# Kernel optimization log

Hardware: AMD Instinct MI355X
Metric: run time of the kernel (lower is better)

The kernel has to match this reference:

```python
import jax, jax.numpy as jnp
import numpy as np

D_MODEL = 1024
NUM_HEADS = 16
D_K = D_MODEL // NUM_HEADS
LN_EPS = 1e-5


def setup_inputs() -> dict:
    key = jax.random.key(0)
    ks = jax.random.split(key, 13)
    B, S, D = 2, 2048, D_MODEL
    s = 1.0 / np.sqrt(D)
    return {
        "query": jax.random.normal(ks[0], (B, S, D), jnp.float32),
        "key": jax.random.normal(ks[1], (B, S, D), jnp.float32),
        "value": jax.random.normal(ks[2], (B, S, D), jnp.float32),
        "Wq": jax.random.normal(ks[3], (D, D), jnp.float32) * s,
        "bq": jnp.zeros((D,), jnp.float32),
        "Wk": jax.random.normal(ks[4], (D, D), jnp.float32) * s,
        "bk": jnp.zeros((D,), jnp.float32),
        "Wv": jax.random.normal(ks[5], (D, D), jnp.float32) * s,
        "bv": jnp.zeros((D,), jnp.float32),
        "Wo": jax.random.normal(ks[6], (D, D), jnp.float32) * s,
        "bo": jnp.zeros((D,), jnp.float32),
        "gamma": jnp.ones((D,), jnp.float32),
        "beta": jnp.zeros((D,), jnp.float32),
    }


def _mha(query, key, value, Wq, bq, Wk, bk, Wv, bv, Wo, bo, gamma, beta):
    B, S, D = query.shape
    H, dk = NUM_HEADS, D_K
    # projections (x @ W + b), reshape to [B, H, S, dk]
    Q = (query @ Wq + bq).reshape(B, S, H, dk).transpose(0, 2, 1, 3)
    K = (key @ Wk + bk).reshape(B, S, H, dk).transpose(0, 2, 1, 3)
    V = (value @ Wv + bv).reshape(B, S, H, dk).transpose(0, 2, 1, 3)
    scores = jnp.einsum("bhsd,bhtd->bhst", Q, K) / np.sqrt(dk).astype(np.float32)
    attn = jax.nn.softmax(scores, axis=-1)  # dropout is identity at inference
    ctx = jnp.einsum("bhst,bhtd->bhsd", attn, V)
    ctx = ctx.transpose(0, 2, 1, 3).reshape(B, S, D)
    out = ctx @ Wo + bo
    # residual + LayerNorm
    x = out + query
    mu = jnp.mean(x, axis=-1, keepdims=True)
    var = jnp.mean(jnp.square(x - mu), axis=-1, keepdims=True)
    y = (x - mu) / jnp.sqrt(var + LN_EPS) * gamma + beta
    return y, attn


def reference(query, key, value, Wq, bq, Wk, bk, Wv, bv, Wo, bo, gamma, beta):
    return _mha(query, key, value, Wq, bq, Wk, bk, Wv, bv, Wo, bo, gamma, beta)
```

## Files before the change

kernel.cpp:

```cpp
#include <hip/hip_runtime.h>
#include <stdint.h>

typedef __attribute__((ext_vector_type(8))) short bf16x8;
typedef __attribute__((ext_vector_type(4))) float f32x4;
typedef unsigned short u16;

#define DEVINL static __device__ __forceinline__

namespace {
constexpr int kS = 2048, kD = 1024, kH = 16, kDK = 64;
constexpr int kBS = 4096, kBH = 32;
constexpr float kEps = 1e-5f;
constexpr float kQScale = 0.125f * 1.44269504088896340736f;
}

DEVINL u16 f2bf(float f) {
  union { float f; unsigned u; } v; v.f = f;
  unsigned r = v.u + 0x7fffu + ((v.u >> 16) & 1u);
  return (u16)(r >> 16);
}
DEVINL float bf2f(u16 us) {
  union { unsigned u; float f; } v; v.u = ((unsigned)us) << 16; return v.f;
}
DEVINL f32x4 mfma16(bf16x8 a, bf16x8 b, f32x4 c) {
  return __builtin_amdgcn_mfma_f32_16x16x32_bf16(a, b, c, 0, 0, 0);
}

__global__ __launch_bounds__(256, 4)
void k_cvt_x(const float* __restrict__ xq, const float* __restrict__ xk,
             const float* __restrict__ xv, u16* __restrict__ oq,
             u16* __restrict__ ok, u16* __restrict__ ov) {
  const int z = blockIdx.y;
  const float* __restrict__ src = (z == 0) ? xq : (z == 1) ? xk : xv;
  u16* __restrict__ dst = (z == 0) ? oq : (z == 1) ? ok : ov;
  const size_t idx = (size_t)blockIdx.x * 256 + threadIdx.x;
  const float4 a = *reinterpret_cast<const float4*>(&src[idx * 8]);
  const float4 b = *reinterpret_cast<const float4*>(&src[idx * 8 + 4]);
  u16 pk[8] = {f2bf(a.x), f2bf(a.y), f2bf(a.z), f2bf(a.w),
               f2bf(b.x), f2bf(b.y), f2bf(b.z), f2bf(b.w)};
  *reinterpret_cast<bf16x8*>(&dst[idx * 8]) =
      *reinterpret_cast<const bf16x8*>(pk);
}

__global__ __launch_bounds__(256, 4)
void k_cvt_w(const float* __restrict__ wq, const float* __restrict__ wk,
             const float* __restrict__ wv, const float* __restrict__ wo,
             u16* __restrict__ oq, u16* __restrict__ ok,
             u16* __restrict__ ov, u16* __restrict__ oo) {
  const int z = blockIdx.z;
  const float* __restrict__ W = (z == 0) ? wq : (z == 1) ? wk : (z == 2) ? wv : wo;
  u16* __restrict__ Wt = (z == 0) ? oq : (z == 1) ? ok : (z == 2) ? ov : oo;
  const int n0 = blockIdx.x * 64, k0 = blockIdx.y * 64;
  const int tid = threadIdx.x;
  __shared__ u16 Tl[64][65];
#pragma unroll
  for (int p = 0; p < 4; ++p) {
    const int idx = tid + p * 256;
    const int kr = idx >> 4, cg = (idx & 15) * 4;
    const float4 v = *reinterpret_cast<const float4*>(&W[(size_t)(k0 + kr) * kD + n0 + cg]);
    Tl[kr][cg + 0] = f2bf(v.x);
    Tl[kr][cg + 1] = f2bf(v.y);
    Tl[kr][cg + 2] = f2bf(v.z);
    Tl[kr][cg + 3] = f2bf(v.w);
  }
  __syncthreads();
  const int n = tid >> 2, kc = (tid & 3) * 16;
  u16 buf[16];
#pragma unroll
  for (int i = 0; i < 16; ++i) buf[i] = Tl[kc + i][n];
  *reinterpret_cast<bf16x8*>(&Wt[(size_t)(n0 + n) * kD + k0 + kc]) =
      *reinterpret_cast<const bf16x8*>(&buf[0]);
  *reinterpret_cast<bf16x8*>(&Wt[(size_t)(n0 + n) * kD + k0 + kc + 8]) =
      *reinterpret_cast<const bf16x8*>(&buf[8]);
}

__global__ __launch_bounds__(256, 2)
void k_proj(const u16* __restrict__ Xq, const u16* __restrict__ Xk,
            const u16* __restrict__ Xv, const u16* __restrict__ Wtq,
            const u16* __restrict__ Wtk, const u16* __restrict__ Wtv,
            const float* __restrict__ bq, const float* __restrict__ bk,
            const float* __restrict__ bv, u16* __restrict__ Qo,
            u16* __restrict__ Ko, u16* __restrict__ Vo) {
  const int which = blockIdx.z;
  const u16* __restrict__ X = (which == 0) ? Xq : (which == 1) ? Xk : Xv;
  const u16* __restrict__ Wt = (which == 0) ? Wtq : (which == 1) ? Wtk : Wtv;
  const float* __restrict__ bias = (which == 0) ? bq : (which == 1) ? bk : bv;
  const float os = (which == 0) ? kQScale : 1.0f;

  const int n0 = blockIdx.x * 128, m0 = blockIdx.y * 128;
  const int tid = threadIdx.x, w = tid >> 6, l = tid & 63;

  __shared__ u16 Al[128][72];
  __shared__ u16 Bl[128][72];

  f32x4 acc[2][8];
#pragma unroll
  for (int i = 0; i < 2; ++i)
#pragma unroll
    for (int j = 0; j < 8; ++j) acc[i][j] = f32x4{0.f, 0.f, 0.f, 0.f};

  for (int k0 = 0; k0 < kD; k0 += 64) {
    __syncthreads();
#pragma unroll
    for (int p = 0; p < 4; ++p) {
      const int idx = tid + p * 256;
      const int row = idx >> 3, c = (idx & 7) * 8;
      *reinterpret_cast<bf16x8*>(&Al[row][c]) =
          *reinterpret_cast<const bf16x8*>(&X[(size_t)(m0 + row) * kD + k0 + c]);
      *reinterpret_cast<bf16x8*>(&Bl[row][c]) =
          *reinterpret_cast<const bf16x8*>(&Wt[(size_t)(n0 + row) * kD + k0 + c]);
    }
    __syncthreads();
#pragma unroll
    for (int k0i = 0; k0i < 64; k0i += 32) {
      const int kk = k0i + (l >> 4) * 8;
      bf16x8 a[2], b[8];
#pragma unroll
      for (int mi = 0; mi < 2; ++mi)
        a[mi] = *reinterpret_cast<const bf16x8*>(&Al[w * 32 + mi * 16 + (l & 15)][kk]);
#pragma unroll
      for (int nj = 0; nj < 8; ++nj)
        b[nj] = *reinterpret_cast<const bf16x8*>(&Bl[nj * 16 + (l & 15)][kk]);
#pragma unroll
      for (int mi = 0; mi < 2; ++mi)
#pragma unroll
        for (int nj = 0; nj < 8; ++nj)
          acc[mi][nj] = mfma16(a[mi], b[nj], acc[mi][nj]);
    }
  }

  u16* __restrict__ Out = (which == 0) ? Qo : (which == 1) ? Ko : Vo;
#pragma unroll
  for (int mi = 0; mi < 2; ++mi)
#pragma unroll
    for (int nj = 0; nj < 8; ++nj) {
      const int col = n0 + nj * 16 + (l & 15);
      const int h = col >> 6, d = col & 63;
      const float bvv = bias[col];
      const int row0 = m0 + w * 32 + mi * 16 + (l >> 4) * 4;
      if (which == 2) {
        const int b_ = row0 >> 11, s0 = row0 & 2047;
        alignas(8) u16 pk[4];
#pragma unroll
        for (int r = 0; r < 4; ++r) pk[r] = f2bf(acc[mi][nj][r] + bvv);
        *reinterpret_cast<uint64_t*>(
            &Out[((size_t)(b_ * kH + h) * kDK + d) * kS + s0]) =
            *reinterpret_cast<const uint64_t*>(pk);
      } else {
#pragma unroll
        for (int r = 0; r < 4; ++r) {
          const int row = row0 + r;
          const int b_ = row >> 11, s_ = row & 2047;
          Out[((size_t)(b_ * kH + h) * kS + s_) * kDK + d] =
              f2bf((acc[mi][nj][r] + bvv) * os);
        }
      }
    }
}

__global__ __launch_bounds__(256, 2)
void k_attn(const u16* __restrict__ Qw, const u16* __restrict__ Kw,
            const u16* __restrict__ Vtw, float* __restrict__ attn_out,
            u16* __restrict__ ctx_out) {
  const int q0 = blockIdx.x * 128;
  const int bh = blockIdx.y;
  const int tid = threadIdx.x, w = tid >> 6, l = tid & 63;
  const int l15 = l & 15, lh = l >> 4;

  __shared__ u16 Qs[128][72];
  __shared__ u16 Ksh[2][64][72];
  __shared__ u16 Vsh[2][64][72];
  __shared__ u16 Ps[128][72];

  const u16* __restrict__ Qg = Qw + ((size_t)bh * kS + q0) * kDK;
  const u16* __restrict__ Kg = Kw + (size_t)bh * kS * kDK;
  const u16* __restrict__ Vtg = Vtw + (size_t)bh * kDK * kS;

#pragma unroll
  for (int p = 0; p < 4; ++p) {
    const int idx = tid + p * 256;
    const int row = idx >> 3, c = (idx & 7) * 8;
    *reinterpret_cast<bf16x8*>(&Qs[row][c]) =
        *reinterpret_cast<const bf16x8*>(&Qg[(size_t)row * kDK + c]);
  }
  bf16x8 kreg[2], vreg[2];
#pragma unroll
  for (int p = 0; p < 2; ++p) {
    const int idx = tid + p * 256;
    const int row = idx >> 3, c = (idx & 7) * 8;
    kreg[p] = *reinterpret_cast<const bf16x8*>(&Kg[(size_t)row * kDK + c]);
  }
#pragma unroll
  for (int p = 0; p < 2; ++p) {
    const int idx = tid + p * 256;
    const int row = idx >> 3, c = (idx & 7) * 8;
    *reinterpret_cast<bf16x8*>(&Ksh[0][row][c]) = kreg[p];
  }
  __syncthreads();

  bf16x8 qf[2][2];
#pragma unroll
  for (int mi = 0; mi < 2; ++mi)
#pragma unroll
    for (int kq = 0; kq < 2; ++kq)
      qf[mi][kq] = *reinterpret_cast<const bf16x8*>(
          &Qs[w * 32 + mi * 16 + l15][kq * 32 + lh * 8]);

  float lsum[2] = {0.f, 0.f};
  int cur = 0;
  for (int t = 0; t < 32; ++t) {
    if (t + 1 < 32) {
      const u16* __restrict__ src = Kg + (size_t)(t + 1) * 64 * kDK;
#pragma unroll
      for (int p = 0; p < 2; ++p) {
        const int idx = tid + p * 256;
        const int row = idx >> 3, c = (idx & 7) * 8;
        kreg[p] = *reinterpret_cast<const bf16x8*>(&src[(size_t)row * kDK + c]);
      }
    }
    f32x4 sacc[2][4];
#pragma unroll
    for (int mi = 0; mi < 2; ++mi)
#pragma unroll
      for (int nj = 0; nj < 4; ++nj) sacc[mi][nj] = f32x4{0.f, 0.f, 0.f, 0.f};
#pragma unroll
    for (int kq = 0; kq < 2; ++kq) {
      const int kk = kq * 32 + lh * 8;
      bf16x8 kf[4];
#pragma unroll
      for (int nj = 0; nj < 4; ++nj)
        kf[nj] = *reinterpret_cast<const bf16x8*>(&Ksh[cur][nj * 16 + l15][kk]);
#pragma unroll
      for (int mi = 0; mi < 2; ++mi)
#pragma unroll
        for (int nj = 0; nj < 4; ++nj)
          sacc[mi][nj] = mfma16(kf[nj], qf[mi][kq], sacc[mi][nj]);
    }
#pragma unroll
    for (int mi = 0; mi < 2; ++mi) {
      float s0 = 0.f;
#pragma unroll
      for (int nj = 0; nj < 4; ++nj)
#pragma unroll
        for (int r = 0; r < 4; ++r) s0 += exp2f(sacc[mi][nj][r]);
      lsum[mi] += s0;
    }
    if (t + 1 < 32) {
#pragma unroll
      for (int p = 0; p < 2; ++p) {
        const int idx = tid + p * 256;
        const int row = idx >> 3, c = (idx & 7) * 8;
        *reinterpret_cast<bf16x8*>(&Ksh[cur ^ 1][row][c]) = kreg[p];
      }
    }
    __syncthreads();
    cur ^= 1;
  }

  float lg[2];
#pragma unroll
  for (int mi = 0; mi < 2; ++mi) {
    float lv = lsum[mi];
    lv += __shfl_xor(lv, 16, 64);
    lv += __shfl_xor(lv, 32, 64);
    lg[mi] = -log2f(lv);
  }

  f32x4 oacc[2][4];
#pragma unroll
  for (int mi = 0; mi < 2; ++mi)
#pragma unroll
    for (int ni = 0; ni < 4; ++ni) oacc[mi][ni] = f32x4{0.f, 0.f, 0.f, 0.f};

  float* __restrict__ attn_base =
      attn_out + (size_t)bh * kS * kS + (size_t)q0 * kS;

#pragma unroll
  for (int p = 0; p < 2; ++p) {
    const int idx = tid + p * 256;
    const int row = idx >> 3, c = (idx & 7) * 8;
    kreg[p] = *reinterpret_cast<const bf16x8*>(&Kg[(size_t)row * kDK + c]);
    vreg[p] = *reinterpret_cast<const bf16x8*>(&Vtg[(size_t)row * kS + c]);
  }
#pragma unroll
  for (int p = 0; p < 2; ++p) {
    const int idx = tid + p * 256;
    const int row = idx >> 3, c = (idx & 7) * 8;
    *reinterpret_cast<bf16x8*>(&Ksh[0][row][c]) = kreg[p];
    *reinterpret_cast<bf16x8*>(&Vsh[0][row][c]) = vreg[p];
  }
  __syncthreads();
  cur = 0;

  for (int t = 0; t < 32; ++t) {
    const int t0 = t * 64;
    if (t + 1 < 32) {
      const u16* __restrict__ ksrc = Kg + (size_t)(t0 + 64) * kDK;
#pragma unroll
      for (int p = 0; p < 2; ++p) {
        const int idx = tid + p * 256;
        const int row = idx >> 3, c = (idx & 7) * 8;
        kreg[p] = *reinterpret_cast<const bf16x8*>(&ksrc[(size_t)row * kDK + c]);
        vreg[p] = *reinterpret_cast<const bf16x8*>(&Vtg[(size_t)row * kS + t0 + 64 + c]);
      }
    }
    f32x4 sacc[2][4];
#pragma unroll
    for (int mi = 0; mi < 2; ++mi)
#pragma unroll
      for (int nj = 0; nj < 4; ++nj) sacc[mi][nj] = f32x4{0.f, 0.f, 0.f, 0.f};
#pragma unroll
    for (int kq = 0; kq < 2; ++kq) {
      const int kk = kq * 32 + lh * 8;
      bf16x8 kf[4];
#pragma unroll
      for (int nj = 0; nj < 4; ++nj)
        kf[nj] = *reinterpret_cast<const bf16x8*>(&Ksh[cur][nj * 16 + l15][kk]);
#pragma unroll
      for (int mi = 0; mi < 2; ++mi)
#pragma unroll
        for (int nj = 0; nj < 4; ++nj)
          sacc[mi][nj] = mfma16(kf[nj], qf[mi][kq], sacc[mi][nj]);
    }
#pragma unroll
    for (int mi = 0; mi < 2; ++mi) {
      const int q = w * 32 + mi * 16 + l15;
#pragma unroll
      for (int nj = 0; nj < 4; ++nj) {
        alignas(8) u16 pk[4];
#pragma unroll
        for (int r = 0; r < 4; ++r)
          pk[r] = f2bf(exp2f(sacc[mi][nj][r] + lg[mi]));
        *reinterpret_cast<uint64_t*>(&Ps[q][nj * 16 + lh * 4]) =
            *reinterpret_cast<const uint64_t*>(pk);
      }
    }
    __syncthreads();
    {
      const int r0 = tid >> 2, c0 = (tid & 3) * 16;
#pragma unroll
      for (int rh = 0; rh < 128; rh += 64) {
        const int row = r0 + rh;
        const bf16x8 x0 = *reinterpret_cast<const bf16x8*>(&Ps[row][c0]);
        const bf16x8 x1 = *reinterpret_cast<const bf16x8*>(&Ps[row][c0 + 8]);
        float* __restrict__ dst = &attn_base[(size_t)row * kS + t0 + c0];
        float4 f0, f1, f2, f3;
        f0.x = bf2f((u16)x0[0]); f0.y = bf2f((u16)x0[1]);
        f0.z = bf2f((u16)x0[2]); f0.w = bf2f((u16)x0[3]);
        f1.x = bf2f((u16)x0[4]); f1.y = bf2f((u16)x0[5]);
        f1.z = bf2f((u16)x0[6]); f1.w = bf2f((u16)x0[7]);
        f2.x = bf2f((u16)x1[0]); f2.y = bf2f((u16)x1[1]);
        f2.z = bf2f((u16)x1[2]); f2.w = bf2f((u16)x1[3]);
        f3.x = bf2f((u16)x1[4]); f3.y = bf2f((u16)x1[5]);
        f3.z = bf2f((u16)x1[6]); f3.w = bf2f((u16)x1[7]);
        *reinterpret_cast<float4*>(dst + 0) = f0;
        *reinterpret_cast<float4*>(dst + 4) = f1;
        *reinterpret_cast<float4*>(dst + 8) = f2;
        *reinterpret_cast<float4*>(dst + 12) = f3;
      }
    }
#pragma unroll
    for (int kq = 0; kq < 2; ++kq) {
      const int kk = kq * 32 + lh * 8;
      bf16x8 pa[2], vb[4];
#pragma unroll
      for (int mi = 0; mi < 2; ++mi)
        pa[mi] = *reinterpret_cast<const bf16x8*>(&Ps[w * 32 + mi * 16 + l15][kk]);
#pragma unroll
      for (int ni = 0; ni < 4; ++ni)
        vb[ni] = *reinterpret_cast<const bf16x8*>(&Vsh[cur][ni * 16 + l15][kk]);
#pragma unroll
      for (int mi = 0; mi < 2; ++mi)
#pragma unroll
        for (int ni = 0; ni < 4; ++ni)
          oacc[mi][ni] = mfma16(pa[mi], vb[ni], oacc[mi][ni]);
    }
    if (t + 1 < 32) {
#pragma unroll
      for (int p = 0; p < 2; ++p) {
        const int idx = tid + p * 256;
        const int row = idx >> 3, c = (idx & 7) * 8;
        *reinterpret_cast<bf16x8*>(&Ksh[cur ^ 1][row][c]) = kreg[p];
        *reinterpret_cast<bf16x8*>(&Vsh[cur ^ 1][row][c]) = vreg[p];
      }
    }
    __syncthreads();
    cur ^= 1;
  }

  const int b_ = bh >> 4, h = bh & 15;
#pragma unroll
  for (int mi = 0; mi < 2; ++mi)
#pragma unroll
    for (int ni = 0; ni < 4; ++ni) {
      const int d = ni * 16 + l15;
#pragma unroll
      for (int r = 0; r < 4; ++r) {
        const int s_ = q0 + w * 32 + mi * 16 + lh * 4 + r;
        ctx_out[((size_t)(b_ * kS + s_)) * kD + h * kDK + d] =
            f2bf(oacc[mi][ni][r]);
      }
    }
}

__global__ __launch_bounds__(256, 2)
void k_oproj(const u16* __restrict__ Cw, const u16* __restrict__ Wto,
             const float* __restrict__ bo, const float* __restrict__ query,
             float* __restrict__ Xout) {
  const int n0 = blockIdx.x * 128, m0 = blockIdx.y * 128;
  const int tid = threadIdx.x, w = tid >> 6, l = tid & 63;

  __shared__ u16 Al[128][72];
  __shared__ u16 Bl[128][72];

  f32x4 acc[2][8];
#pragma unroll
  for (int i = 0; i < 2; ++i)
#pragma unroll
    for (int j = 0; j < 8; ++j) acc[i][j] = f32x4{0.f, 0.f, 0.f, 0.f};

  for (int k0 = 0; k0 < kD; k0 += 64) {
    __syncthreads();
#pragma unroll
    for (int p = 0; p < 4; ++p) {
      const int idx = tid + p * 256;
      const int row = idx >> 3, c = (idx & 7) * 8;
      *reinterpret_cast<bf16x8*>(&Al[row][c]) =
          *reinterpret_cast<const bf16x8*>(&Cw[(size_t)(m0 + row) * kD + k0 + c]);
      *reinterpret_cast<bf16x8*>(&Bl[row][c]) =
          *reinterpret_cast<const bf16x8*>(&Wto[(size_t)(n0 + row) * kD + k0 + c]);
    }
    __syncthreads();
#pragma unroll
    for (int k0i = 0; k0i < 64; k0i += 32) {
      const int kk = k0i + (l >> 4) * 8;
      bf16x8 a[2], b[8];
#pragma unroll
      for (int mi = 0; mi < 2; ++mi)
        a[mi] = *reinterpret_cast<const bf16x8*>(&Al[w * 32 + mi * 16 + (l & 15)][kk]);
#pragma unroll
      for (int nj = 0; nj < 8; ++nj)
        b[nj] = *reinterpret_cast<const bf16x8*>(&Bl[nj * 16 + (l & 15)][kk]);
#pragma unroll
      for (int mi = 0; mi < 2; ++mi)
#pragma unroll
        for (int nj = 0; nj < 8; ++nj)
          acc[mi][nj] = mfma16(a[mi], b[nj], acc[mi][nj]);
    }
  }

#pragma unroll
  for (int mi = 0; mi < 2; ++mi)
#pragma unroll
    for (int nj = 0; nj < 8; ++nj) {
      const int col = n0 + nj * 16 + (l & 15);
      const float bvv = bo[col];
#pragma unroll
      for (int r = 0; r < 4; ++r) {
        const int row = m0 + w * 32 + mi * 16 + (l >> 4) * 4 + r;
        Xout[(size_t)row * kD + col] =
            acc[mi][nj][r] + bvv + query[(size_t)row * kD + col];
      }
    }
}

__global__ __launch_bounds__(256, 4)
void k_ln(float* __restrict__ Y, const float* __restrict__ gamma,
          const float* __restrict__ beta) {
  const int row = blockIdx.x;
  float* __restrict__ x = Y + (size_t)row * kD;
  const int tid = threadIdx.x;
  const float4 v = reinterpret_cast<const float4*>(x)[tid];
  float s = v.x + v.y + v.z + v.w;
  float sq = v.x * v.x + v.y * v.y + v.z * v.z + v.w * v.w;
#pragma unroll
  for (int mk = 1; mk < 64; mk <<= 1) {
    s += __shfl_xor(s, mk, 64);
    sq += __shfl_xor(sq, mk, 64);
  }
  __shared__ float ss[4], ssq[4];
  if ((tid & 63) == 0) { ss[tid >> 6] = s; ssq[tid >> 6] = sq; }
  __syncthreads();
  s = ss[0] + ss[1] + ss[2] + ss[3];
  sq = ssq[0] + ssq[1] + ssq[2] + ssq[3];
  const float mu = s * (1.f / kD);
  const float rstd = rsqrtf(sq * (1.f / kD) - mu * mu + kEps);
  const float4 g = reinterpret_cast<const float4*>(gamma)[tid];
  const float4 bb = reinterpret_cast<const float4*>(beta)[tid];
  float4 o;
  o.x = (v.x - mu) * rstd * g.x + bb.x;
  o.y = (v.y - mu) * rstd * g.y + bb.y;
  o.z = (v.z - mu) * rstd * g.z + bb.z;
  o.w = (v.w - mu) * rstd * g.w + bb.w;
  reinterpret_cast<float4*>(x)[tid] = o;
}

extern "C" void kernel_launch(void* const* d_in, const int* in_sizes, int n_in,
                              void* d_out, int out_size, void* d_ws, size_t ws_size,
                              hipStream_t stream) {
  (void)in_sizes; (void)n_in; (void)out_size; (void)ws_size;
  const float* query = (const float*)d_in[0];
  const float* key_i = (const float*)d_in[1];
  const float* value = (const float*)d_in[2];
  const float* Wq = (const float*)d_in[3];
  const float* bq = (const float*)d_in[4];
  const float* Wk = (const float*)d_in[5];
  const float* bk = (const float*)d_in[6];
  const float* Wv = (const float*)d_in[7];
  const float* bv = (const float*)d_in[8];
  const float* Wo = (const float*)d_in[9];
  const float* bo = (const float*)d_in[10];
  const float* gamma = (const float*)d_in[11];
  const float* beta = (const float*)d_in[12];

  float* y_out = (float*)d_out;
  float* attn_out = y_out + (size_t)kBS * kD;

  u16* Xbq = (u16*)d_ws;
  u16* Xbk = Xbq + (size_t)kBS * kD;
  u16* Xbv = Xbk + (size_t)kBS * kD;
  u16* Wtq = Xbv + (size_t)kBS * kD;
  u16* Wtk = Wtq + (size_t)kD * kD;
  u16* Wtv = Wtk + (size_t)kD * kD;
  u16* Wto = Wtv + (size_t)kD * kD;
  u16* Qw  = Wto + (size_t)kD * kD;
  u16* Kw  = Qw + (size_t)kBH * kS * kDK;
  u16* Vtw = Kw + (size_t)kBH * kS * kDK;
  u16* Cw  = Xbq;

  k_cvt_x<<<dim3(2048, 3), 256, 0, stream>>>(query, key_i, value, Xbq, Xbk, Xbv);
  k_cvt_w<<<dim3(16, 16, 4), 256, 0, stream>>>(Wq, Wk, Wv, Wo, Wtq, Wtk, Wtv, Wto);
  k_proj<<<dim3(kD / 128, kBS / 128, 3), 256, 0, stream>>>(
      Xbq, Xbk, Xbv, Wtq, Wtk, Wtv, bq, bk, bv, Qw, Kw, Vtw);
  k_attn<<<dim3(kS / 128, kBH), 256, 0, stream>>>(Qw, Kw, Vtw, attn_out, Cw);
  k_oproj<<<dim3(kD / 128, kBS / 128), 256, 0, stream>>>(Cw, Wto, bo, query, y_out);
  k_ln<<<dim3(kBS), 256, 0, stream>>>(y_out, gamma, beta);
}
```

Measured before the change: 334.2 us.

## Use direct global-to-LDS loads with XOR swizzle and transposed MFMA for vector stores

Replaces register-staged global-to-LDS copies in the projection, attention and output GEMMs with global_load_lds direct transfers, dropping LDS row padding in favour of an XOR swizzle so reads stay bank-conflict free. MFMA operand order is swapped so each lane holds four consecutive columns, which lets the epilogues write 8-byte and 16-byte vectors instead of scattered scalar stores. The attention kernel merges the Q and P shared buffers to cut LDS use, and launch bounds are raised to allow three blocks per CU. Risks include reduced latency hiding, since the K/V prefetch is still single-stage, and register pressure under the tighter occupancy bound.

```diff
diff --git a/kernel.cpp b/kernel.cpp
--- a/kernel.cpp
+++ b/kernel.cpp
@@ -25,6 +25,12 @@
 DEVINL f32x4 mfma16(bf16x8 a, bf16x8 b, f32x4 c) {
   return __builtin_amdgcn_mfma_f32_16x16x32_bf16(a, b, c, 0, 0, 0);
 }
+DEVINL void gl_lds16(const u16* g, u16* l) {
+  __builtin_amdgcn_global_load_lds(
+      (const __attribute__((address_space(1))) void*)(g),
+      (__attribute__((address_space(3))) void*)(l), 16, 0, 0);
+}
+DEVINL int kswz(int kq, int lh, int aswz) { return (((kq << 2) + lh) ^ aswz) << 3; }
 
 __global__ __launch_bounds__(256, 4)
 void k_cvt_x(const float* __restrict__ xq, const float* __restrict__ xk,
@@ -74,7 +80,7 @@
       *reinterpret_cast<const bf16x8*>(&buf[8]);
 }
 
-__global__ __launch_bounds__(256, 2)
+__global__ __launch_bounds__(256, 3)
 void k_proj(const u16* __restrict__ Xq, const u16* __restrict__ Xk,
             const u16* __restrict__ Xv, const u16* __restrict__ Wtq,
             const u16* __restrict__ Wtk, const u16* __restrict__ Wtv,
@@ -85,13 +91,14 @@
   const u16* __restrict__ X = (which == 0) ? Xq : (which == 1) ? Xk : Xv;
   const u16* __restrict__ Wt = (which == 0) ? Wtq : (which == 1) ? Wtk : Wtv;
   const float* __restrict__ bias = (which == 0) ? bq : (which == 1) ? bk : bv;
-  const float os = (which == 0) ? kQScale : 1.0f;
 
   const int n0 = blockIdx.x * 128, m0 = blockIdx.y * 128;
   const int tid = threadIdx.x, w = tid >> 6, l = tid & 63;
-
-  __shared__ u16 Al[128][72];
-  __shared__ u16 Bl[128][72];
+  const int l15 = l & 15, lh = l >> 4;
+  const int aswz = l15 & 7;
+
+  __shared__ u16 Al[128][64];
+  __shared__ u16 Bl[128][64];
 
   f32x4 acc[2][8];
 #pragma unroll
@@ -103,62 +110,84 @@
     __syncthreads();
 #pragma unroll
     for (int p = 0; p < 4; ++p) {
-      const int idx = tid + p * 256;
-      const int row = idx >> 3, c = (idx & 7) * 8;
-      *reinterpret_cast<bf16x8*>(&Al[row][c]) =
-          *reinterpret_cast<const bf16x8*>(&X[(size_t)(m0 + row) * kD + k0 + c]);
-      *reinterpret_cast<bf16x8*>(&Bl[row][c]) =
-          *reinterpret_cast<const bf16x8*>(&Wt[(size_t)(n0 + row) * kD + k0 + c]);
-    }
-    __syncthreads();
-#pragma unroll
-    for (int k0i = 0; k0i < 64; k0i += 32) {
-      const int kk = k0i + (l >> 4) * 8;
+      const int slot = p * 256 + tid;
+      const int row = slot >> 3;
+      const int k8 = (slot & 7) ^ (row & 7);
+      gl_lds16(&X[(size_t)(m0 + row) * kD + k0 + k8 * 8],
+               &Al[0][0] + (size_t)(p * 256 + w * 64) * 8);
+      gl_lds16(&Wt[(size_t)(n0 + row) * kD + k0 + k8 * 8],
+               &Bl[0][0] + (size_t)(p * 256 + w * 64) * 8);
+    }
+    __syncthreads();
+#pragma unroll
+    for (int kq = 0; kq < 2; ++kq) {
+      const int kk = kswz(kq, lh, aswz);
       bf16x8 a[2], b[8];
 #pragma unroll
       for (int mi = 0; mi < 2; ++mi)
-        a[mi] = *reinterpret_cast<const bf16x8*>(&Al[w * 32 + mi * 16 + (l & 15)][kk]);
+        a[mi] = *reinterpret_cast<const bf16x8*>(&Al[w * 32 + mi * 16 + l15][kk]);
 #pragma unroll
       for (int nj = 0; nj < 8; ++nj)
-        b[nj] = *reinterpret_cast<const bf16x8*>(&Bl[nj * 16 + (l & 15)][kk]);
-#pragma unroll
-      for (int mi = 0; mi < 2; ++mi)
-#pragma unroll
-        for (int nj = 0; nj < 8; ++nj)
-          acc[mi][nj] = mfma16(a[mi], b[nj], acc[mi][nj]);
-    }
-  }
-
-  u16* __restrict__ Out = (which == 0) ? Qo : (which == 1) ? Ko : Vo;
-#pragma unroll
-  for (int mi = 0; mi < 2; ++mi)
-#pragma unroll
-    for (int nj = 0; nj < 8; ++nj) {
-      const int col = n0 + nj * 16 + (l & 15);
-      const int h = col >> 6, d = col & 63;
-      const float bvv = bias[col];
-      const int row0 = m0 + w * 32 + mi * 16 + (l >> 4) * 4;
+        b[nj] = *reinterpret_cast<const bf16x8*>(&Bl[nj * 16 + l15][kk]);
       if (which == 2) {
+#pragma unroll
+        for (int mi = 0; mi < 2; ++mi)
+#pragma unroll
+          for (int nj = 0; nj < 8; ++nj)
+            acc[mi][nj] = mfma16(a[mi], b[nj], acc[mi][nj]);
+      } else {
+#pragma unroll
+        for (int mi = 0; mi < 2; ++mi)
+#pragma unroll
+          for (int nj = 0; nj < 8; ++nj)
+            acc[mi][nj] = mfma16(b[nj], a[mi], acc[mi][nj]);
+      }
+    }
+  }
+
+  if (which == 2) {
+#pragma unroll
+    for (int mi = 0; mi < 2; ++mi)
+#pragma unroll
+      for (int nj = 0; nj < 8; ++nj) {
+        const int col = n0 + nj * 16 + l15;
+        const int h = col >> 6, d = col & 63;
+        const float bvv = bias[col];
+        const int row0 = m0 + w * 32 + mi * 16 + lh * 4;
         const int b_ = row0 >> 11, s0 = row0 & 2047;
         alignas(8) u16 pk[4];
 #pragma unroll
         for (int r = 0; r < 4; ++r) pk[r] = f2bf(acc[mi][nj][r] + bvv);
         *reinterpret_cast<uint64_t*>(
-            &Out[((size_t)(b_ * kH + h) * kDK + d) * kS + s0]) =
+            &Vo[((size_t)(b_ * kH + h) * kDK + d) * kS + s0]) =
             *reinterpret_cast<const uint64_t*>(pk);
-      } else {
-#pragma unroll
-        for (int r = 0; r < 4; ++r) {
-          const int row = row0 + r;
-          const int b_ = row >> 11, s_ = row & 2047;
-          Out[((size_t)(b_ * kH + h) * kS + s_) * kDK + d] =
-              f2bf((acc[mi][nj][r] + bvv) * os);
-        }
-      }
-    }
-}
-
-__global__ __launch_bounds__(256, 2)
+      }
+  } else {
+    u16* __restrict__ Out = (which == 0) ? Qo : Ko;
+    const float os = (which == 0) ? kQScale : 1.0f;
+#pragma unroll
+    for (int mi = 0; mi < 2; ++mi) {
+      const int srow = m0 + w * 32 + mi * 16 + l15;
+      const int b_ = srow >> 11, s_ = srow & 2047;
+#pragma unroll
+      for (int nj = 0; nj < 8; ++nj) {
+        const int c0 = n0 + nj * 16 + lh * 4;
+        const int h = c0 >> 6, d0 = c0 & 63;
+        const float4 b4 = *reinterpret_cast<const float4*>(&bias[c0]);
+        alignas(8) u16 pk[4];
+        pk[0] = f2bf((acc[mi][nj][0] + b4.x) * os);
+        pk[1] = f2bf((acc[mi][nj][1] + b4.y) * os);
+        pk[2] = f2bf((acc[mi][nj][2] + b4.z) * os);
+        pk[3] = f2bf((acc[mi][nj][3] + b4.w) * os);
+        *reinterpret_cast<uint64_t*>(
+            &Out[((size_t)(b_ * kH + h) * kS + s_) * kDK + d0]) =
+            *reinterpret_cast<const uint64_t*>(pk);
+      }
+    }
+  }
+}
+
+__global__ __launch_bounds__(256, 3)
 void k_attn(const u16* __restrict__ Qw, const u16* __restrict__ Kw,
             const u16* __restrict__ Vtw, float* __restrict__ attn_out,
             u16* __restrict__ ctx_out) {
@@ -166,11 +195,11 @@
   const int bh = blockIdx.y;
   const int tid = threadIdx.x, w = tid >> 6, l = tid & 63;
   const int l15 = l & 15, lh = l >> 4;
-
-  __shared__ u16 Qs[128][72];
-  __shared__ u16 Ksh[2][64][72];
-  __shared__ u16 Vsh[2][64][72];
-  __shared__ u16 Ps[128][72];
+  const int aswz = l15 & 7;
+
+  __shared__ u16 PQs[128][72];
+  __shared__ u16 Ksh[2][64][64];
+  __shared__ u16 Vsh[2][64][64];
 
   const u16* __restrict__ Qg = Qw + ((size_t)bh * kS + q0) * kDK;
   const u16* __restrict__ Kg = Kw + (size_t)bh * kS * kDK;
@@ -180,21 +209,15 @@
   for (int p = 0; p < 4; ++p) {
     const int idx = tid + p * 256;
     const int row = idx >> 3, c = (idx & 7) * 8;
-    *reinterpret_cast<bf16x8*>(&Qs[row][c]) =
+    *reinterpret_cast<bf16x8*>(&PQs[row][c]) =
         *reinterpret_cast<const bf16x8*>(&Qg[(size_t)row * kDK + c]);
   }
-  bf16x8 kreg[2], vreg[2];
 #pragma unroll
   for (int p = 0; p < 2; ++p) {
-    const int idx = tid + p * 256;
-    const int row = idx >> 3, c = (idx & 7) * 8;
-    kreg[p] = *reinterpret_cast<const bf16x8*>(&Kg[(size_t)row * kDK + c]);
-  }
-#pragma unroll
-  for (int p = 0; p < 2; ++p) {
-    const int idx = tid + p * 256;
-    const int row = idx >> 3, c = (idx & 7) * 8;
-    *reinterpret_cast<bf16x8*>(&Ksh[0][row][c]) = kreg[p];
+    const int slot = p * 256 + tid;
+    const int row = slot >> 3, k8 = (slot & 7) ^ (row & 7);
+    gl_lds16(&Kg[(size_t)row * kDK + k8 * 8],
+             &Ksh[0][0][0] + (size_t)(p * 256 + w * 64) * 8);
   }
   __syncthreads();
 
@@ -204,18 +227,19 @@
 #pragma unroll
     for (int kq = 0; kq < 2; ++kq)
       qf[mi][kq] = *reinterpret_cast<const bf16x8*>(
-          &Qs[w * 32 + mi * 16 + l15][kq * 32 + lh * 8]);
+          &PQs[w * 32 + mi * 16 + l15][kq * 32 + lh * 8]);
 
   float lsum[2] = {0.f, 0.f};
-  int cur = 0;
   for (int t = 0; t < 32; ++t) {
+    const int buf = t & 1;
     if (t + 1 < 32) {
       const u16* __restrict__ src = Kg + (size_t)(t + 1) * 64 * kDK;
 #pragma unroll
       for (int p = 0; p < 2; ++p) {
-        const int idx = tid + p * 256;
-        const int row = idx >> 3, c = (idx & 7) * 8;
-        kreg[p] = *reinterpret_cast<const bf16x8*>(&src[(size_t)row * kDK + c]);
+        const int slot = p * 256 + tid;
+        const int row = slot >> 3, k8 = (slot & 7) ^ (row & 7);
+        gl_lds16(&src[(size_t)row * kDK + k8 * 8],
+                 &Ksh[buf ^ 1][0][0] + (size_t)(p * 256 + w * 64) * 8);
       }
     }
     f32x4 sacc[2][4];
@@ -225,11 +249,11 @@
       for (int nj = 0; nj < 4; ++nj) sacc[mi][nj] = f32x4{0.f, 0.f, 0.f, 0.f};
 #pragma unroll
     for (int kq = 0; kq < 2; ++kq) {
-      const int kk = kq * 32 + lh * 8;
+      const int kk = kswz(kq, lh, aswz);
       bf16x8 kf[4];
 #pragma unroll
       for (int nj = 0; nj < 4; ++nj)
-        kf[nj] = *reinterpret_cast<const bf16x8*>(&Ksh[cur][nj * 16 + l15][kk]);
+        kf[nj] = *reinterpret_cast<const bf16x8*>(&Ksh[buf][nj * 16 + l15][kk]);
 #pragma unroll
       for (int mi = 0; mi < 2; ++mi)
 #pragma unroll
@@ -245,16 +269,7 @@
         for (int r = 0; r < 4; ++r) s0 += exp2f(sacc[mi][nj][r]);
       lsum[mi] += s0;
     }
-    if (t + 1 < 32) {
-#pragma unroll
-      for (int p = 0; p < 2; ++p) {
-        const int idx = tid + p * 256;
-        const int row = idx >> 3, c = (idx & 7) * 8;
-        *reinterpret_cast<bf16x8*>(&Ksh[cur ^ 1][row][c]) = kreg[p];
-      }
-    }
-    __syncthreads();
-    cur ^= 1;
+    __syncthreads();
   }
 
   float lg[2];
@@ -277,31 +292,27 @@
 
 #pragma unroll
   for (int p = 0; p < 2; ++p) {
-    const int idx = tid + p * 256;
-    const int row = idx >> 3, c = (idx & 7) * 8;
-    kreg[p] = *reinterpret_cast<const bf16x8*>(&Kg[(size_t)row * kDK + c]);
-    vreg[p] = *reinterpret_cast<const bf16x8*>(&Vtg[(size_t)row * kS + c]);
-  }
-#pragma unroll
-  for (int p = 0; p < 2; ++p) {
-    const int idx = tid + p * 256;
-    const int row = idx >> 3, c = (idx & 7) * 8;
-    *reinterpret_cast<bf16x8*>(&Ksh[0][row][c]) = kreg[p];
-    *reinterpret_cast<bf16x8*>(&Vsh[0][row][c]) = vreg[p];
+    const int slot = p * 256 + tid;
+    const int row = slot >> 3, k8 = (slot & 7) ^ (row & 7);
+    gl_lds16(&Kg[(size_t)row * kDK + k8 * 8],
+             &Ksh[0][0][0] + (size_t)(p * 256 + w * 64) * 8);
+    gl_lds16(&Vtg[(size_t)row * kS + k8 * 8],
+             &Vsh[0][0][0] + (size_t)(p * 256 + w * 64) * 8);
   }
   __syncthreads();
-  cur = 0;
 
   for (int t = 0; t < 32; ++t) {
+    const int buf = t & 1;
     const int t0 = t * 64;
     if (t + 1 < 32) {
-      const u16* __restrict__ ksrc = Kg + (size_t)(t0 + 64) * kDK;
 #pragma unroll
       for (int p = 0; p < 2; ++p) {
-        const int idx = tid + p * 256;
-        const int row = idx >> 3, c = (idx & 7) * 8;
-        kreg[p] = *reinterpret_cast<const bf16x8*>(&ksrc[(size_t)row * kDK + c]);
-        vreg[p] = *reinterpret_cast<const bf16x8*>(&Vtg[(size_t)row * kS + t0 + 64 + c]);
+        const int slot = p * 256 + tid;
+        const int row = slot >> 3, k8 = (slot & 7) ^ (row & 7);
+        gl_lds16(&Kg[(size_t)(t0 + 64 + row) * kDK + k8 * 8],
+                 &Ksh[buf ^ 1][0][0] + (size_t)(p * 256 + w * 64) * 8);
+        gl_lds16(&Vtg[(size_t)row * kS + t0 + 64 + k8 * 8],
+                 &Vsh[buf ^ 1][0][0] + (size_t)(p * 256 + w * 64) * 8);
       }
     }
     f32x4 sacc[2][4];
@@ -311,11 +322,11 @@
       for (int nj = 0; nj < 4; ++nj) sacc[mi][nj] = f32x4{0.f, 0.f, 0.f, 0.f};
 #pragma unroll
     for (int kq = 0; kq < 2; ++kq) {
-      const int kk = kq * 32 + lh * 8;
+      const int kk = kswz(kq, lh, aswz);
       bf16x8 kf[4];
 #pragma unroll
       for (int nj = 0; nj < 4; ++nj)
-        kf[nj] = *reinterpret_cast<const bf16x8*>(&Ksh[cur][nj * 16 + l15][kk]);
+        kf[nj] = *reinterpret_cast<const bf16x8*>(&Ksh[buf][nj * 16 + l15][kk]);
 #pragma unroll
       for (int mi = 0; mi < 2; ++mi)
 #pragma unroll
@@ -331,7 +342,7 @@
 #pragma unroll
         for (int r = 0; r < 4; ++r)
           pk[r] = f2bf(exp2f(sacc[mi][nj][r] + lg[mi]));
-        *reinterpret_cast<uint64_t*>(&Ps[q][nj * 16 + lh * 4]) =
+        *reinterpret_cast<uint64_t*>(&PQs[q][nj * 16 + lh * 4]) =
             *reinterpret_cast<const uint64_t*>(pk);
       }
     }
@@ -341,8 +352,8 @@
 #pragma unroll
       for (int rh = 0; rh < 128; rh += 64) {
         const int row = r0 + rh;
-        const bf16x8 x0 = *reinterpret_cast<const bf16x8*>(&Ps[row][c0]);
-        const bf16x8 x1 = *reinterpret_cast<const bf16x8*>(&Ps[row][c0 + 8]);
+        const bf16x8 x0 = *reinterpret_cast<const bf16x8*>(&PQs[row][c0]);
+        const bf16x8 x1 = *reinterpret_cast<const bf16x8*>(&PQs[row][c0 + 8]);
         float* __restrict__ dst = &attn_base[(size_t)row * kS + t0 + c0];
         float4 f0, f1, f2, f3;
         f0.x = bf2f((u16)x0[0]); f0.y = bf2f((u16)x0[1]);
@@ -361,57 +372,52 @@
     }
 #pragma unroll
     for (int kq = 0; kq < 2; ++kq) {
-      const int kk = kq * 32 + lh * 8;
+      const int kk = kswz(kq, lh, aswz);
+      const int kkp = kq * 32 + lh * 8;
       bf16x8 pa[2], vb[4];
 #pragma unroll
       for (int mi = 0; mi < 2; ++mi)
-        pa[mi] = *reinterpret_cast<const bf16x8*>(&Ps[w * 32 + mi * 16 + l15][kk]);
+        pa[mi] = *reinterpret_cast<const bf16x8*>(&PQs[w * 32 + mi * 16 + l15][kkp]);
 #pragma unroll
       for (int ni = 0; ni < 4; ++ni)
-        vb[ni] = *reinterpret_cast<const bf16x8*>(&Vsh[cur][ni * 16 + l15][kk]);
+        vb[ni] = *reinterpret_cast<const bf16x8*>(&Vsh[buf][ni * 16 + l15][kk]);
 #pragma unroll
       for (int mi = 0; mi < 2; ++mi)
 #pragma unroll
         for (int ni = 0; ni < 4; ++ni)
-          oacc[mi][ni] = mfma16(pa[mi], vb[ni], oacc[mi][ni]);
-    }
-    if (t + 1 < 32) {
-#pragma unroll
-      for (int p = 0; p < 2; ++p) {
-        const int idx = tid + p * 256;
-        const int row = idx >> 3, c = (idx & 7) * 8;
-        *reinterpret_cast<bf16x8*>(&Ksh[cur ^ 1][row][c]) = kreg[p];
-        *reinterpret_cast<bf16x8*>(&Vsh[cur ^ 1][row][c]) = vreg[p];
-      }
-    }
-    __syncthreads();
-    cur ^= 1;
+          oacc[mi][ni] = mfma16(vb[ni], pa[mi], oacc[mi][ni]);
+    }
+    __syncthreads();
   }
 
   const int b_ = bh >> 4, h = bh & 15;
 #pragma unroll
-  for (int mi = 0; mi < 2; ++mi)
+  for (int mi = 0; mi < 2; ++mi) {
+    const int s_ = q0 + w * 32 + mi * 16 + l15;
 #pragma unroll
     for (int ni = 0; ni < 4; ++ni) {
-      const int d = ni * 16 + l15;
-#pragma unroll
-      for (int r = 0; r < 4; ++r) {
-        const int s_ = q0 + w * 32 + mi * 16 + lh * 4 + r;
-        ctx_out[((size_t)(b_ * kS + s_)) * kD + h * kDK + d] =
-            f2bf(oacc[mi][ni][r]);
-      }
-    }
-}
-
-__global__ __launch_bounds__(256, 2)
+      const int d0 = ni * 16 + lh * 4;
+      alignas(8) u16 pk[4];
+#pragma unroll
+      for (int r = 0; r < 4; ++r) pk[r] = f2bf(oacc[mi][ni][r]);
+      *reinterpret_cast<uint64_t*>(
+          &ctx_out[((size_t)(b_ * kS + s_)) * kD + h * kDK + d0]) =
+          *reinterpret_cast<const uint64_t*>(pk);
+    }
+  }
+}
+
+__global__ __launch_bounds__(256, 3)
 void k_oproj(const u16* __restrict__ Cw, const u16* __restrict__ Wto,
              const float* __restrict__ bo, const float* __restrict__ query,
              float* __restrict__ Xout) {
   const int n0 = blockIdx.x * 128, m0 = blockIdx.y * 128;
   const int tid = threadIdx.x, w = tid >> 6, l = tid & 63;
-
-  __shared__ u16 Al[128][72];
-  __shared__ u16 Bl[128][72];
+  const int l15 = l & 15, lh = l >> 4;
+  const int aswz = l15 & 7;
+
+  __shared__ u16 Al[128][64];
+  __shared__ u16 Bl[128][64];
 
   f32x4 acc[2][8];
 #pragma unroll
@@ -423,45 +429,49 @@
     __syncthreads();
 #pragma unroll
     for (int p = 0; p < 4; ++p) {
-      const int idx = tid + p * 256;
-      const int row = idx >> 3, c = (idx & 7) * 8;
-      *reinterpret_cast<bf16x8*>(&Al[row][c]) =
-          *reinterpret_cast<const bf16x8*>(&Cw[(size_t)(m0 + row) * kD + k0 + c]);
-      *reinterpret_cast<bf16x8*>(&Bl[row][c]) =
-          *reinterpret_cast<const bf16x8*>(&Wto[(size_t)(n0 + row) * kD + k0 + c]);
-    }
-    __syncthreads();
-#pragma unroll
-    for (int k0i = 0; k0i < 64; k0i += 32) {
-      const int kk = k0i + (l >> 4) * 8;
+      const int slot = p * 256 + tid;
+      const int row = slot >> 3;
+      const int k8 = (slot & 7) ^ (row & 7);
+      gl_lds16(&Cw[(size_t)(m0 + row) * kD + k0 + k8 * 8],
+               &Al[0][0] + (size_t)(p * 256 + w * 64) * 8);
+      gl_lds16(&Wto[(size_t)(n0 + row) * kD + k0 + k8 * 8],
+               &Bl[0][0] + (size_t)(p * 256 + w * 64) * 8);
+    }
+    __syncthreads();
+#pragma unroll
+    for (int kq = 0; kq < 2; ++kq) {
+      const int kk = kswz(kq, lh, aswz);
       bf16x8 a[2], b[8];
 #pragma unroll
       for (int mi = 0; mi < 2; ++mi)
-        a[mi] = *reinterpret_cast<const bf16x8*>(&Al[w * 32 + mi * 16 + (l & 15)][kk]);
+        a[mi] = *reinterpret_cast<const bf16x8*>(&Al[w * 32 + mi * 16 + l15][kk]);
 #pragma unroll
       for (int nj = 0; nj < 8; ++nj)
-        b[nj] = *reinterpret_cast<const bf16x8*>(&Bl[nj * 16 + (l & 15)][kk]);
+        b[nj] = *reinterpret_cast<const bf16x8*>(&Bl[nj * 16 + l15][kk]);
 #pragma unroll
       for (int mi = 0; mi < 2; ++mi)
 #pragma unroll
         for (int nj = 0; nj < 8; ++nj)
-          acc[mi][nj] = mfma16(a[mi], b[nj], acc[mi][nj]);
-    }
-  }
-
-#pragma unroll
-  for (int mi = 0; mi < 2; ++mi)
+          acc[mi][nj] = mfma16(b[nj], a[mi], acc[mi][nj]);
+    }
+  }
+
+#pragma unroll
+  for (int mi = 0; mi < 2; ++mi) {
+    const int row = m0 + w * 32 + mi * 16 + l15;
 #pragma unroll
     for (int nj = 0; nj < 8; ++nj) {
-      const int col = n0 + nj * 16 + (l & 15);
-      const float bvv = bo[col];
-#pragma unroll
-      for (int r = 0; r < 4; ++r) {
-        const int row = m0 + w * 32 + mi * 16 + (l >> 4) * 4 + r;
-        Xout[(size_t)row * kD + col] =
-            acc[mi][nj][r] + bvv + query[(size_t)row * kD + col];
-      }
-    }
+      const int c0 = n0 + nj * 16 + lh * 4;
+      const float4 b4 = *reinterpret_cast<const float4*>(&bo[c0]);
+      const float4 q4 = *reinterpret_cast<const float4*>(&query[(size_t)row * kD + c0]);
+      float4 o;
+      o.x = acc[mi][nj][0] + b4.x + q4.x;
+      o.y = acc[mi][nj][1] + b4.y + q4.y;
+      o.z = acc[mi][nj][2] + b4.z + q4.z;
+      o.w = acc[mi][nj][3] + b4.w + q4.w;
+      *reinterpret_cast<float4*>(&Xout[(size_t)row * kD + c0]) = o;
+    }
+  }
 }
 
 __global__ __launch_bounds__(256, 4)
```

Measured after the change: 427.8 us. 28.0% more time.
